# Performance work log

Measured on AMD Instinct MI355X. Metric: run time of the kernel, lower is better.

The kernel has to match this reference:

```python
import jax, jax.numpy as jnp
import numpy as np

OUT_F, IN_F = 4096, 11008
NUMEL = OUT_F * IN_F            # divisible by 256
NUM_SUPER = NUMEL // 256        # super-blocks of 8 sub-blocks x 32 values


def setup_inputs() -> dict:
    key = jax.random.key(0)
    k = jax.random.split(key, 7)
    x = jax.random.normal(k[0], (64, IN_F), dtype=jnp.float32)
    packed = jax.random.randint(k[1], (NUMEL // 2,), 0, 256, dtype=jnp.int32)
    d = jax.random.uniform(k[2], (NUM_SUPER,), dtype=jnp.float32) * 0.02
    dmin = jax.random.uniform(k[3], (NUM_SUPER,), dtype=jnp.float32) * 0.02
    scales = jax.random.randint(k[4], (NUM_SUPER * 8,), 0, 64, dtype=jnp.int32)
    mins = jax.random.randint(k[5], (NUM_SUPER * 8,), 0, 64, dtype=jnp.int32)
    bias = jax.random.normal(k[6], (OUT_F,), dtype=jnp.float32) * 0.02
    return {"x": x, "packed": packed, "d": d, "dmin": dmin,
            "scales": scales, "mins": mins, "bias": bias}


def _dequant_q4k(packed, d, dmin, scales, mins):
    # unpack two 4-bit quants per byte, interleaved low/high (stack dim=1 + flatten)
    low = packed & 15
    high = (packed >> 4) & 15
    q = jnp.stack([low, high], axis=1).reshape(NUM_SUPER, 8, 32).astype(jnp.float32)
    sc = (scales.astype(jnp.float32) / 63.0).reshape(NUM_SUPER, 8, 1)
    mn = (mins.astype(jnp.float32) / 63.0).reshape(NUM_SUPER, 8, 1)
    normalized = q / 15.0 * sc + mn
    w = normalized * d.reshape(NUM_SUPER, 1, 1) + dmin.reshape(NUM_SUPER, 1, 1)
    return w.reshape(OUT_F, IN_F)


def reference(x, packed, d, dmin, scales, mins, bias):
    w = _dequant_q4k(packed, d, dmin, scales, mins)   # [OUT_F, IN_F] fp32
    return x @ w.T + bias                              # F.linear
```

## Files before the change

kernel.cpp:

```cpp
#include <hip/hip_runtime.h>
#include <stdint.h>

#define OUT_F   4096
#define IN_F    11008
#define BATCH   64
#define NSUP    43
#define SB_ROW  344
#define IPR     5504
#define NKS     16
#define NCB     32
#define XP_BYTES   (344 * 256 * 16)
#define SCMN_BYTES (NSUP * 4096 * 16)
#define DDM_BYTES  (NSUP * 4096 * 8)
#define PART_OFF   (XP_BYTES + SCMN_BYTES + DDM_BYTES)
#define PART_BYTES ((size_t)NKS * BATCH * OUT_F * 4)
#define WS_FULL    (PART_OFF + PART_BYTES)

typedef __attribute__((ext_vector_type(8))) short  short8;
typedef __attribute__((ext_vector_type(4))) float  floatx4;
typedef __attribute__((ext_vector_type(4))) int    intx4;

__device__ __forceinline__ unsigned pack_bf16(float f0, float f1) {
    return __builtin_amdgcn_perm(__float_as_uint(f1), __float_as_uint(f0), 0x07060302u);
}

__global__ __launch_bounds__(256) void xprep_kernel(const float* __restrict__ x,
                                                    intx4* __restrict__ xp) {
    const int ksb = blockIdx.x;
    const int mt  = threadIdx.x >> 6;
    const int l   = threadIdx.x & 63;
    const int lo  = l & 15, hi = l >> 4;
    const float* src = x + (mt * 16 + lo) * IN_F + ksb * 32 + hi * 8;
    floatx4 a0 = *(const floatx4*)src;
    floatx4 a1 = *(const floatx4*)(src + 4);
    intx4 r;
    r.x = pack_bf16(a0.x, a0.y);
    r.y = pack_bf16(a0.z, a0.w);
    r.z = pack_bf16(a1.x, a1.y);
    r.w = pack_bf16(a1.z, a1.w);
    xp[(mt * 344 + ksb) * 64 + l] = r;
}

__global__ __launch_bounds__(256) void scprep_kernel(const int* __restrict__ scales,
                                                     const int* __restrict__ mins,
                                                     const float* __restrict__ dd,
                                                     const float* __restrict__ dmn,
                                                     intx4* __restrict__ scmn_p,
                                                     float2* __restrict__ ddm_p) {
    const int tg  = blockIdx.x * 256 + threadIdx.x;
    const int row = tg / 43;
    const int sup = tg - row * 43;
    const intx4 s0 = *(const intx4*)(scales + row * SB_ROW + sup * 8);
    const intx4 s1 = *(const intx4*)(scales + row * SB_ROW + sup * 8 + 4);
    const intx4 m0 = *(const intx4*)(mins   + row * SB_ROW + sup * 8);
    const intx4 m1 = *(const intx4*)(mins   + row * SB_ROW + sup * 8 + 4);
    intx4 o;
    o.x = s0.x | (s0.y << 8) | (s0.z << 16) | (s0.w << 24);
    o.y = s1.x | (s1.y << 8) | (s1.z << 16) | (s1.w << 24);
    o.z = m0.x | (m0.y << 8) | (m0.z << 16) | (m0.w << 24);
    o.w = m1.x | (m1.y << 8) | (m1.z << 16) | (m1.w << 24);
    scmn_p[sup * 4096 + row] = o;
    float2 dp;
    dp.x = dd[row * NSUP + sup];
    dp.y = dmn[row * NSUP + sup];
    ddm_p[sup * 4096 + row] = dp;
}

__global__ __launch_bounds__(256) void init_out_kernel(const float* __restrict__ bias,
                                                       float* __restrict__ out) {
    int i = blockIdx.x * 256 + threadIdx.x;
    out[i] = bias[i & (OUT_F - 1)];
}

__global__ __launch_bounds__(256) void reduce_kernel(const float* __restrict__ part,
                                                     const float* __restrict__ bias,
                                                     float* __restrict__ out) {
    const int i = blockIdx.x * 256 + threadIdx.x;
    float s = bias[i & (OUT_F - 1)];
    #pragma unroll
    for (int k = 0; k < NKS; ++k) s += part[(size_t)k * (BATCH * OUT_F) + i];
    out[i] = s;
}

template<bool USE_PART>
__global__ __launch_bounds__(256, 2) void qlin_main(
    const intx4*  __restrict__ xp,
    const int*    __restrict__ packed,
    const intx4*  __restrict__ scmn_p,
    const float2* __restrict__ ddm_p,
    float*        __restrict__ part,
    float*        __restrict__ out)
{
    __shared__ intx4  xfs[2][2048];
    __shared__ intx4  scs[2][128];
    __shared__ float2 dds[2][128];

    const int ks  = blockIdx.x & 15;
    const int nb  = blockIdx.x >> 4;
    const int tid = threadIdx.x;
    const int w   = tid >> 6;
    const int l   = tid & 63;
    const int lo  = l & 15, hi = l >> 4;

    const int sup0 = ks < 11 ? 3 * ks : 33 + 2 * (ks - 11);
    const int nsup = ks < 11 ? 3 : 2;

    const int o0 = nb * 128 + (2 * w) * 16 + lo;
    const int o1 = o0 + 16;
    const int* bpA0 = packed + o0 * IPR + hi * 4;
    const int* bpA1 = packed + o1 * IPR + hi * 4;

    floatx4 acc[4][2];
    #pragma unroll
    for (int mt = 0; mt < 4; ++mt) { acc[mt][0] = (floatx4)0.0f; acc[mt][1] = (floatx4)0.0f; }

    intx4 xtmp[8]; intx4 sctv; float2 ddv;

    auto stage_issue = [&](int sup) {
        const intx4* xsrc = xp + sup * 512;
        #pragma unroll
        for (int i = 0; i < 8; ++i) {
            const int idx = i * 256 + tid;
            xtmp[i] = xsrc[(idx >> 9) * 22016 + (idx & 511)];
        }
        if (tid < 128) sctv = scmn_p[sup * 4096 + nb * 128 + tid];
        else           ddv  = ddm_p[sup * 4096 + nb * 128 + (tid - 128)];
    };
    auto stage_commit = [&](int b) {
        #pragma unroll
        for (int i = 0; i < 8; ++i) xfs[b][i * 256 + tid] = xtmp[i];
        if (tid < 128) scs[b][tid] = sctv;
        else           dds[b][tid - 128] = ddv;
    };

    struct Half { intx4 v[2][4]; };
    auto load_half = [&](int sup, int half) {
        Half r;
        #pragma unroll
        for (int st = 0; st < 4; ++st) {
            r.v[0][st] = __builtin_nontemporal_load(
                (const intx4*)(bpA0 + sup * 128 + half * 64 + st * 16));
            r.v[1][st] = __builtin_nontemporal_load(
                (const intx4*)(bpA1 + sup * 128 + half * 64 + st * 16));
        }
        return r;
    };

    Half brP = load_half(sup0, 0);
    stage_issue(sup0);
    stage_commit(0);

    #pragma unroll 1
    for (int s = 0; s < nsup; ++s) {
        const int b = s & 1;
        const int sup = sup0 + s;
        __syncthreads();

        if (s + 1 < nsup) stage_issue(sup + 1);
        Half brQ = load_half(sup, 1);
        Half brPn;
        if (s + 1 < nsup) brPn = load_half(sup + 1, 0);

        const intx4  sv0 = scs[b][w * 32 + lo];
        const intx4  sv1 = scs[b][w * 32 + 16 + lo];
        const float2 dp0 = dds[b][w * 32 + lo];
        const float2 dp1 = dds[b][w * 32 + 16 + lo];
        const float a945_0 = dp0.x * (1.0f / 945.0f), a63_0 = dp0.x * (1.0f / 63.0f);
        const float a945_1 = dp1.x * (1.0f / 945.0f), a63_1 = dp1.x * (1.0f / 63.0f);

        auto compute_half = [&](int half, const Half& br) {
            #pragma unroll
            for (int st = 0; st < 4; ++st) {
                const int step = half * 4 + st;
                intx4 x0 = xfs[b][0 * 512 + step * 64 + l];
                intx4 x1 = xfs[b][1 * 512 + step * 64 + l];
                intx4 x2 = xfs[b][2 * 512 + step * 64 + l];
                intx4 x3 = xfs[b][3 * 512 + step * 64 + l];
                #pragma unroll
                for (int nt = 0; nt < 2; ++nt) {
                    const intx4 sv = nt ? sv1 : sv0;
                    const int scw = half ? sv.y : sv.x;
                    const int mnw = half ? sv.w : sv.z;
                    const float A = (nt ? a945_1 : a945_0) * (float)((scw >> (st * 8)) & 255);
                    const float B = fmaf((nt ? a63_1 : a63_0),
                                         (float)((mnw >> (st * 8)) & 255),
                                         (nt ? dp1.y : dp0.y));
                    const intx4 bv = br.v[nt][st];
                    union { intx4 i; short8 s8; } uw;
                    uw.i.x = pack_bf16(fmaf((float)(bv.x & 15), A, B),
                                       fmaf((float)(bv.x >> 4), A, B));
                    uw.i.y = pack_bf16(fmaf((float)(bv.y & 15), A, B),
                                       fmaf((float)(bv.y >> 4), A, B));
                    uw.i.z = pack_bf16(fmaf((float)(bv.z & 15), A, B),
                                       fmaf((float)(bv.z >> 4), A, B));
                    uw.i.w = pack_bf16(fmaf((float)(bv.w & 15), A, B),
                                       fmaf((float)(bv.w >> 4), A, B));
                    union { intx4 i; short8 s8; } u0, u1, u2, u3;
                    u0.i = x0; u1.i = x1; u2.i = x2; u3.i = x3;
                    acc[0][nt] = __builtin_amdgcn_mfma_f32_16x16x32_bf16(u0.s8, uw.s8, acc[0][nt], 0, 0, 0);
                    acc[1][nt] = __builtin_amdgcn_mfma_f32_16x16x32_bf16(u1.s8, uw.s8, acc[1][nt], 0, 0, 0);
                    acc[2][nt] = __builtin_amdgcn_mfma_f32_16x16x32_bf16(u2.s8, uw.s8, acc[2][nt], 0, 0, 0);
                    acc[3][nt] = __builtin_amdgcn_mfma_f32_16x16x32_bf16(u3.s8, uw.s8, acc[3][nt], 0, 0, 0);
                }
            }
        };

        compute_half(0, brP);
        compute_half(1, brQ);

        if (s + 1 < nsup) { stage_commit(1 - b); brP = brPn; }
    }

    if (USE_PART) {
        float* p0 = part + (size_t)ks * (BATCH * OUT_F);
        #pragma unroll
        for (int mt = 0; mt < 4; ++mt) {
            #pragma unroll
            for (int r = 0; r < 4; ++r) {
                const int row = (mt * 16 + hi * 4 + r) * OUT_F;
                p0[row + o0] = acc[mt][0][r];
                p0[row + o1] = acc[mt][1][r];
            }
        }
    } else {
        #pragma unroll
        for (int mt = 0; mt < 4; ++mt) {
            #pragma unroll
            for (int r = 0; r < 4; ++r) {
                const int row = (mt * 16 + hi * 4 + r) * OUT_F;
                atomicAdd(out + row + o0, acc[mt][0][r]);
                atomicAdd(out + row + o1, acc[mt][1][r]);
            }
        }
    }
}

extern "C" void kernel_launch(void* const* d_in, const int* in_sizes, int n_in,
                              void* d_out, int out_size, void* d_ws, size_t ws_size,
                              hipStream_t stream) {
    (void)in_sizes; (void)n_in; (void)out_size;
    const float* x      = (const float*)d_in[0];
    const int*   packed = (const int*)d_in[1];
    const float* d      = (const float*)d_in[2];
    const float* dmin   = (const float*)d_in[3];
    const int*   scales = (const int*)d_in[4];
    const int*   mins   = (const int*)d_in[5];
    const float* bias   = (const float*)d_in[6];
    float* out = (float*)d_out;

    intx4*  xp     = (intx4*)d_ws;
    intx4*  scmn_p = (intx4*)((char*)d_ws + XP_BYTES);
    float2* ddm_p  = (float2*)((char*)d_ws + XP_BYTES + SCMN_BYTES);
    float*  part   = (float*)((char*)d_ws + PART_OFF);
    const bool has_part = ws_size >= (size_t)WS_FULL;

    xprep_kernel<<<344, 256, 0, stream>>>(x, xp);
    scprep_kernel<<<688, 256, 0, stream>>>(scales, mins, d, dmin, scmn_p, ddm_p);

    if (has_part) {
        qlin_main<true><<<NCB * NKS, 256, 0, stream>>>(
            xp, packed, scmn_p, ddm_p, part, out);
        reduce_kernel<<<(BATCH * OUT_F) / 256, 256, 0, stream>>>(part, bias, out);
    } else {
        init_out_kernel<<<(BATCH * OUT_F) / 256, 256, 0, stream>>>(bias, out);
        qlin_main<false><<<NCB * NKS, 256, 0, stream>>>(
            xp, packed, scmn_p, ddm_p, part, out);
    }
}
```

Before: 168.2 us.

## Merge prep kernels and restructure main-loop staging and weight prefetch

Fuses the x-conversion and scale-packing prep kernels into one launch to drop a kernel launch. In the main kernel, the next superblock's x/scale staging is now loaded and written to the other LDS buffer immediately rather than deferred past compute, and the next first-half weight prefetch is moved between the two compute halves to lower register pressure. Weight loads switch from nontemporal to ordinary loads. The changes trade some load latency hiding for fewer live registers, and may alter cache behaviour for the streamed weights.

```diff
diff --git a/kernel.cpp b/kernel.cpp
--- a/kernel.cpp
+++ b/kernel.cpp
@@ -24,46 +24,47 @@
     return __builtin_amdgcn_perm(__float_as_uint(f1), __float_as_uint(f0), 0x07060302u);
 }
 
-__global__ __launch_bounds__(256) void xprep_kernel(const float* __restrict__ x,
-                                                    intx4* __restrict__ xp) {
-    const int ksb = blockIdx.x;
-    const int mt  = threadIdx.x >> 6;
-    const int l   = threadIdx.x & 63;
-    const int lo  = l & 15, hi = l >> 4;
-    const float* src = x + (mt * 16 + lo) * IN_F + ksb * 32 + hi * 8;
-    floatx4 a0 = *(const floatx4*)src;
-    floatx4 a1 = *(const floatx4*)(src + 4);
-    intx4 r;
-    r.x = pack_bf16(a0.x, a0.y);
-    r.y = pack_bf16(a0.z, a0.w);
-    r.z = pack_bf16(a1.x, a1.y);
-    r.w = pack_bf16(a1.z, a1.w);
-    xp[(mt * 344 + ksb) * 64 + l] = r;
-}
-
-__global__ __launch_bounds__(256) void scprep_kernel(const int* __restrict__ scales,
-                                                     const int* __restrict__ mins,
-                                                     const float* __restrict__ dd,
-                                                     const float* __restrict__ dmn,
-                                                     intx4* __restrict__ scmn_p,
-                                                     float2* __restrict__ ddm_p) {
-    const int tg  = blockIdx.x * 256 + threadIdx.x;
-    const int row = tg / 43;
-    const int sup = tg - row * 43;
-    const intx4 s0 = *(const intx4*)(scales + row * SB_ROW + sup * 8);
-    const intx4 s1 = *(const intx4*)(scales + row * SB_ROW + sup * 8 + 4);
-    const intx4 m0 = *(const intx4*)(mins   + row * SB_ROW + sup * 8);
-    const intx4 m1 = *(const intx4*)(mins   + row * SB_ROW + sup * 8 + 4);
-    intx4 o;
-    o.x = s0.x | (s0.y << 8) | (s0.z << 16) | (s0.w << 24);
-    o.y = s1.x | (s1.y << 8) | (s1.z << 16) | (s1.w << 24);
-    o.z = m0.x | (m0.y << 8) | (m0.z << 16) | (m0.w << 24);
-    o.w = m1.x | (m1.y << 8) | (m1.z << 16) | (m1.w << 24);
-    scmn_p[sup * 4096 + row] = o;
-    float2 dp;
-    dp.x = dd[row * NSUP + sup];
-    dp.y = dmn[row * NSUP + sup];
-    ddm_p[sup * 4096 + row] = dp;
+__global__ __launch_bounds__(256) void prep_kernel(const float* __restrict__ x,
+                                                   const int* __restrict__ scales,
+                                                   const int* __restrict__ mins,
+                                                   const float* __restrict__ dd,
+                                                   const float* __restrict__ dmn,
+                                                   intx4* __restrict__ xp,
+                                                   intx4* __restrict__ scmn_p,
+                                                   float2* __restrict__ ddm_p) {
+    if (blockIdx.x < 344) {
+        const int ksb = blockIdx.x;
+        const int mt  = threadIdx.x >> 6;
+        const int l   = threadIdx.x & 63;
+        const int lo  = l & 15, hi = l >> 4;
+        const float* src = x + (mt * 16 + lo) * IN_F + ksb * 32 + hi * 8;
+        floatx4 a0 = *(const floatx4*)src;
+        floatx4 a1 = *(const floatx4*)(src + 4);
+        intx4 r;
+        r.x = pack_bf16(a0.x, a0.y);
+        r.y = pack_bf16(a0.z, a0.w);
+        r.z = pack_bf16(a1.x, a1.y);
+        r.w = pack_bf16(a1.z, a1.w);
+        xp[(mt * 344 + ksb) * 64 + l] = r;
+    } else {
+        const int tg  = (blockIdx.x - 344) * 256 + threadIdx.x;
+        const int row = tg / 43;
+        const int sup = tg - row * 43;
+        const intx4 s0 = *(const intx4*)(scales + row * SB_ROW + sup * 8);
+        const intx4 s1 = *(const intx4*)(scales + row * SB_ROW + sup * 8 + 4);
+        const intx4 m0 = *(const intx4*)(mins   + row * SB_ROW + sup * 8);
+        const intx4 m1 = *(const intx4*)(mins   + row * SB_ROW + sup * 8 + 4);
+        intx4 o;
+        o.x = s0.x | (s0.y << 8) | (s0.z << 16) | (s0.w << 24);
+        o.y = s1.x | (s1.y << 8) | (s1.z << 16) | (s1.w << 24);
+        o.z = m0.x | (m0.y << 8) | (m0.z << 16) | (m0.w << 24);
+        o.w = m1.x | (m1.y << 8) | (m1.z << 16) | (m1.w << 24);
+        scmn_p[sup * 4096 + row] = o;
+        float2 dp;
+        dp.x = dd[row * NSUP + sup];
+        dp.y = dmn[row * NSUP + sup];
+        ddm_p[sup * 4096 + row] = dp;
+    }
 }
 
 __global__ __launch_bounds__(256) void init_out_kernel(const float* __restrict__ bias,
@@ -114,19 +115,17 @@
     #pragma unroll
     for (int mt = 0; mt < 4; ++mt) { acc[mt][0] = (floatx4)0.0f; acc[mt][1] = (floatx4)0.0f; }
 
-    intx4 xtmp[8]; intx4 sctv; float2 ddv;
-
-    auto stage_issue = [&](int sup) {
+    auto stage = [&](int sup, int b) {
+        intx4 xtmp[8];
         const intx4* xsrc = xp + sup * 512;
         #pragma unroll
         for (int i = 0; i < 8; ++i) {
             const int idx = i * 256 + tid;
             xtmp[i] = xsrc[(idx >> 9) * 22016 + (idx & 511)];
         }
+        intx4 sctv; float2 ddv;
         if (tid < 128) sctv = scmn_p[sup * 4096 + nb * 128 + tid];
         else           ddv  = ddm_p[sup * 4096 + nb * 128 + (tid - 128)];
-    };
-    auto stage_commit = [&](int b) {
         #pragma unroll
         for (int i = 0; i < 8; ++i) xfs[b][i * 256 + tid] = xtmp[i];
         if (tid < 128) scs[b][tid] = sctv;
@@ -138,17 +137,14 @@
         Half r;
         #pragma unroll
         for (int st = 0; st < 4; ++st) {
-            r.v[0][st] = __builtin_nontemporal_load(
-                (const intx4*)(bpA0 + sup * 128 + half * 64 + st * 16));
-            r.v[1][st] = __builtin_nontemporal_load(
-                (const intx4*)(bpA1 + sup * 128 + half * 64 + st * 16));
+            r.v[0][st] = *(const intx4*)(bpA0 + sup * 128 + half * 64 + st * 16);
+            r.v[1][st] = *(const intx4*)(bpA1 + sup * 128 + half * 64 + st * 16);
         }
         return r;
     };
 
+    stage(sup0, 0);
     Half brP = load_half(sup0, 0);
-    stage_issue(sup0);
-    stage_commit(0);
 
     #pragma unroll 1
     for (int s = 0; s < nsup; ++s) {
@@ -156,10 +152,8 @@
         const int sup = sup0 + s;
         __syncthreads();
 
-        if (s + 1 < nsup) stage_issue(sup + 1);
+        if (s + 1 < nsup) stage(sup + 1, 1 - b);
         Half brQ = load_half(sup, 1);
-        Half brPn;
-        if (s + 1 < nsup) brPn = load_half(sup + 1, 0);
 
         const intx4  sv0 = scs[b][w * 32 + lo];
         const intx4  sv1 = scs[b][w * 32 + 16 + lo];
@@ -206,9 +200,8 @@
         };
 
         compute_half(0, brP);
+        if (s + 1 < nsup) brP = load_half(sup + 1, 0);
         compute_half(1, brQ);
-
-        if (s + 1 < nsup) { stage_commit(1 - b); brP = brPn; }
     }
 
     if (USE_PART) {
@@ -254,8 +247,7 @@
     float*  part   = (float*)((char*)d_ws + PART_OFF);
     const bool has_part = ws_size >= (size_t)WS_FULL;
 
-    xprep_kernel<<<344, 256, 0, stream>>>(x, xp);
-    scprep_kernel<<<688, 256, 0, stream>>>(scales, mins, d, dmin, scmn_p, ddm_p);
+    prep_kernel<<<344 + 688, 256, 0, stream>>>(x, scales, mins, d, dmin, xp, scmn_p, ddm_p);
 
     if (has_part) {
         qlin_main<true><<<NCB * NKS, 256, 0, stream>>>(
```

After: 173.8 us. +3.3%, slower.
